# Optimization experiments

Hardware: AMD Instinct MI355X
Metric: run time of the kernel (lower is better)

The kernel has to match this reference:

```python
import jax, jax.numpy as jnp
import numpy as np

B, S, H, HKV, D = 1, 1024, 32, 8, 128
HID = H * D
GROUPS = H // HKV
ALPHA_K, ALPHA_V = 0.5, 0.5
GAMMA_MIN, GAMMA_MAX = 0.5, 2.0
ETA_MIN, ETA_MAX = 0.5, 2.0
BETA_BIAS, BIAS_CAP = 1.0, 5.0
BETA_POST = 0.5
ROPE_THETA = 10000.0


def setup_inputs() -> dict:
    key = jax.random.key(0)
    ks = jax.random.split(key, 9)
    hidden_states = jax.random.normal(ks[0], (B, S, HID), jnp.float32) * 0.02
    # additive causal mask (LLaMA-style, large negative above diagonal)
    causal = jnp.tril(jnp.ones((S, S), dtype=bool))
    attention_mask = jnp.where(causal, 0.0, -1e9).astype(jnp.float32)[None, None]
    position_ids = jnp.arange(S, dtype=jnp.int32)[None]
    sq = 1.0 / np.sqrt(HID)
    Wq = jax.random.normal(ks[1], (HID, HID), jnp.float32) * sq
    Wk = jax.random.normal(ks[2], (HKV * D, HID), jnp.float32) * sq
    Wv = jax.random.normal(ks[3], (HKV * D, HID), jnp.float32) * sq
    Wo = jax.random.normal(ks[4], (HID, HID), jnp.float32) * sq
    prior = jax.random.uniform(ks[5], (S,), jnp.float32)  # per-key-position prior, in [0,1)
    head_mask_l1 = (jax.random.uniform(ks[6], (H,)) > 0.5).astype(jnp.float32)
    head_mask_l2 = (jax.random.uniform(ks[7], (H,)) > 0.5).astype(jnp.float32)
    return {"hidden_states": hidden_states, "attention_mask": attention_mask,
            "position_ids": position_ids, "Wq": Wq, "Wk": Wk, "Wv": Wv, "Wo": Wo,
            "prior": prior, "head_mask_l1": head_mask_l1, "head_mask_l2": head_mask_l2}


def _rope(position_ids):
    inv_freq = 1.0 / (ROPE_THETA ** (jnp.arange(0, D, 2, dtype=jnp.float32) / D))
    freqs = position_ids.astype(jnp.float32)[..., None] * inv_freq  # [B,S,D/2]
    emb = jnp.concatenate([freqs, freqs], axis=-1)                  # [B,S,D]
    return jnp.cos(emb)[:, None], jnp.sin(emb)[:, None]             # [B,1,S,D]


def _rotate_half(x):
    x1, x2 = x[..., : D // 2], x[..., D // 2:]
    return jnp.concatenate([-x2, x1], axis=-1)


def reference(hidden_states, attention_mask, position_ids, Wq, Wk, Wv, Wo,
              prior, head_mask_l1, head_mask_l2):
    b, s, _ = hidden_states.shape
    # projections (Linear without bias: x @ W.T)
    q = (hidden_states @ Wq.T).reshape(b, s, H, D).transpose(0, 2, 1, 3)     # [B,H,S,D]
    k = (hidden_states @ Wk.T).reshape(b, s, HKV, D).transpose(0, 2, 1, 3)   # [B,Hkv,S,D]
    v = (hidden_states @ Wv.T).reshape(b, s, HKV, D).transpose(0, 2, 1, 3)
    cos, sin = _rope(position_ids)
    q = q * cos + _rotate_half(q) * sin
    k = k * cos + _rotate_half(k) * sin
    # repeat_kv: expand KV heads to match query heads (GQA)
    k = jnp.repeat(k, GROUPS, axis=1)  # [B,H,S,D]
    v = jnp.repeat(v, GROUPS, axis=1)
    # level4_scale: per-key-position multiplicative scaling of K and V
    gamma = jnp.clip(1.0 + ALPHA_K * prior, GAMMA_MIN, GAMMA_MAX)  # [S]
    eta = jnp.clip(1.0 + ALPHA_V * prior, ETA_MIN, ETA_MAX)
    k = k * gamma[None, None, :, None]
    v = v * eta[None, None, :, None]
    # attention logits
    attn = jnp.einsum('bhqd,bhkd->bhqk', q, k) / np.sqrt(D)
    # level1_bias: capped additive bias on logits, blended per-head
    bias = jnp.clip(BETA_BIAS * prior, -BIAS_CAP, BIAS_CAP)        # [S] over key dim
    steered = attn + bias[None, None, None, :]
    attn = attn + (steered - attn) * head_mask_l1[None, :, None, None]
    # causal mask
    attn = attn + attention_mask
    probs = jax.nn.softmax(attn.astype(jnp.float32), axis=-1)
    # level2_post: post-softmax rescale + renormalize, blended per-head
    sp = probs * (1.0 + BETA_POST * prior)[None, None, None, :]
    sp = sp / jnp.sum(sp, axis=-1, keepdims=True)
    probs = probs + (sp - probs) * head_mask_l2[None, :, None, None]
    out = jnp.einsum('bhqk,bhkd->bhqd', probs, v)                  # [B,H,S,D]
    out = out.transpose(0, 2, 1, 3).reshape(b, s, HID)
    return out @ Wo.T
```

## Files before the change

### kernel.cpp

```cpp
#include <hip/hip_runtime.h>
#include <math.h>

#define S_LEN 1024
#define HID_DIM 4096
#define NH 32
#define NKV 8
#define DH 128

typedef __attribute__((ext_vector_type(8))) short sh8;
typedef __attribute__((ext_vector_type(4))) short sh4;
typedef __attribute__((ext_vector_type(4))) float f4;

__device__ __forceinline__ unsigned short f2bf(float x) {
    union { float f; unsigned int u; } v; v.f = x;
    unsigned int r = v.u + 0x7FFFu + ((v.u >> 16) & 1u);
    return (unsigned short)(r >> 16);
}

__device__ __forceinline__ void gl_lds16(const unsigned short* g, unsigned short* l) {
    __builtin_amdgcn_global_load_lds(
        (const __attribute__((address_space(1))) unsigned int*)g,
        (__attribute__((address_space(3))) unsigned int*)l, 16, 0, 0);
}


__global__ void cvt_hw(const float* __restrict__ hidden, const float* __restrict__ Wq,
                       const float* __restrict__ Wk, const float* __restrict__ Wv,
                       unsigned short* __restrict__ hbf, unsigned short* __restrict__ wbuf)
{
    const int idx = blockIdx.x * 256 + threadIdx.x;
    const int NH4 = (S_LEN * HID_DIM) / 4;
    float4 v;
    sh4* dst;
    if (idx < NH4) {
        v = ((const float4*)hidden)[idx];
        dst = (sh4*)hbf + idx;
    } else {
        const int j = idx - NH4;
        const int row = j >> 10;
        if (row < 4096)      v = ((const float4*)Wq)[j];
        else if (row < 5120) v = ((const float4*)Wk)[j - 4096 * 1024];
        else                 v = ((const float4*)Wv)[j - 5120 * 1024];
        dst = (sh4*)wbuf + j;
    }
    sh4 o;
    o.x = (short)f2bf(v.x); o.y = (short)f2bf(v.y);
    o.z = (short)f2bf(v.z); o.w = (short)f2bf(v.w);
    *dst = o;
}

__global__ __launch_bounds__(256)
void gemm_t(const unsigned short* __restrict__ A, const unsigned short* __restrict__ B,
            float* __restrict__ C, int K, int ldc)
{
    __shared__ __attribute__((aligned(16))) unsigned short sA[2][2][64 * 32];
    __shared__ __attribute__((aligned(16))) unsigned short sB[2][2][128 * 32];

    const int tid  = threadIdx.x;
    const int wave = tid >> 6;
    const int lane = tid & 63;
    const int l15  = lane & 15;
    const int quad = lane >> 4;
    const int m0   = blockIdx.y * 64;
    const int n0   = blockIdx.x * 128;
    const int wm   = (wave >> 1) * 32;
    const int wn   = (wave & 1) * 64;

    const int sslot = (lane & 7) ^ ((lane >> 3) & 7);
    const int srow  = 2 * (lane >> 3) + (sslot >> 2);
    const int scol  = (sslot & 3) * 8;

    const unsigned short* Ag  = A + (size_t)(m0 + 16 * wave + srow) * K + scol;
    const unsigned short* Bg1 = B + (size_t)(n0 + 16 * wave + srow) * K + scol;
    const unsigned short* Bg2 = B + (size_t)(n0 + 64 + 16 * wave + srow) * K + scol;

    f4 acc[2][4];
#pragma unroll
    for (int i = 0; i < 2; i++)
#pragma unroll
        for (int j = 0; j < 4; j++)
            acc[i][j] = f4{0.0f, 0.0f, 0.0f, 0.0f};

    const int rphys = ((((l15 & 1) << 2) + quad) ^ (l15 >> 1)) * 8;

#pragma unroll
    for (int s = 0; s < 2; s++) {
        gl_lds16(Ag + 32 * s,  &sA[0][s][wave * 512]);
        gl_lds16(Bg1 + 32 * s, &sB[0][s][wave * 512]);
        gl_lds16(Bg2 + 32 * s, &sB[0][s][2048 + wave * 512]);
    }

    for (int k0 = 0; k0 < K; k0 += 64) {
        const int cur = (k0 >> 6) & 1;
        __syncthreads();
        const int k1 = k0 + 64;
        if (k1 < K) {
#pragma unroll
            for (int s = 0; s < 2; s++) {
                gl_lds16(Ag + k1 + 32 * s,  &sA[cur ^ 1][s][wave * 512]);
                gl_lds16(Bg1 + k1 + 32 * s, &sB[cur ^ 1][s][wave * 512]);
                gl_lds16(Bg2 + k1 + 32 * s, &sB[cur ^ 1][s][2048 + wave * 512]);
            }
        }

#pragma unroll
        for (int s = 0; s < 2; s++) {
            sh8 af[2], bf[4];
#pragma unroll
            for (int i = 0; i < 2; i++)
                af[i] = *(const sh8*)(&sA[cur][s][((wm + i * 16 + l15) >> 1) * 64 + rphys]);
#pragma unroll
            for (int j = 0; j < 4; j++)
                bf[j] = *(const sh8*)(&sB[cur][s][((wn + j * 16 + l15) >> 1) * 64 + rphys]);
#pragma unroll
            for (int i = 0; i < 2; i++)
#pragma unroll
                for (int j = 0; j < 4; j++)
                    acc[i][j] = __builtin_amdgcn_mfma_f32_16x16x32_bf16(af[i], bf[j], acc[i][j], 0, 0, 0);
        }
    }

#pragma unroll
    for (int i = 0; i < 2; i++) {
        const int mrow = m0 + wm + i * 16 + quad * 4;
#pragma unroll
        for (int j = 0; j < 4; j++) {
            const int ncol = n0 + wn + j * 16 + l15;
#pragma unroll
            for (int r = 0; r < 4; r++)
                C[(size_t)(mrow + r) * ldc + ncol] = acc[i][j][r];
        }
    }
}

__global__ void prep2(const float* __restrict__ qkv, const int* __restrict__ pos_ids,
                      const float* __restrict__ prior,
                      const float* __restrict__ Wo,
                      unsigned short* __restrict__ Qb, unsigned short* __restrict__ Kb,
                      unsigned short* __restrict__ Vt, float* __restrict__ addvT,
                      unsigned short* __restrict__ Wob)
{
    const int idx = blockIdx.x * blockDim.x + threadIdx.x;
    const int NQ = S_LEN * 40 * 64;
    const int NV = S_LEN * NKV * DH;
    if (idx < NQ) {
        const int s   = idx / (40 * 64);
        const int rem = idx % (40 * 64);
        const int hh  = rem >> 6;
        const int i   = rem & 63;
        const float pos  = (float)pos_ids[s];
        const float invf = exp2f(-13.287712379549449f * (i * 0.015625f));
        const float ph = pos * invf;
        const float c = cosf(ph), sn = sinf(ph);
        if (hh < NH) {
            const float* base = qkv + (size_t)s * 6144 + hh * 128;
            const float x1 = base[i], x2 = base[i + 64];
            const float sc = 0.08838834764831845f * 1.4426950408889634f;
            unsigned short* q = Qb + ((size_t)hh * S_LEN + s) * DH;
            q[i]      = f2bf((x1 * c - x2 * sn) * sc);
            q[i + 64] = f2bf((x2 * c + x1 * sn) * sc);
        } else {
            const int kvh = hh - NH;
            const float* base = qkv + (size_t)s * 6144 + 4096 + kvh * 128;
            const float p = prior[s];
            const float gamma = fminf(fmaxf(1.0f + 0.5f * p, 0.5f), 2.0f);
            const float x1 = base[i], x2 = base[i + 64];
            unsigned short* kp = Kb + ((size_t)kvh * S_LEN + s) * DH;
            kp[i]      = f2bf((x1 * c - x2 * sn) * gamma);
            kp[i + 64] = f2bf((x2 * c + x1 * sn) * gamma);
        }
    } else if (idx < NQ + NV) {
        const int j = idx - NQ;
        const int s   = j / (NKV * DH);
        const int rem = j % (NKV * DH);
        const int kvh = rem >> 7;
        const int d   = rem & 127;
        const float p = prior[s];
        const float eta = fminf(fmaxf(1.0f + 0.5f * p, 0.5f), 2.0f);
        const float val = qkv[(size_t)s * 6144 + 5120 + kvh * 128 + d] * eta;
        Vt[((size_t)kvh * DH + d) * S_LEN + s] = f2bf(val);
    } else {
        const int j2 = idx - NQ - NV;
        if (j2 < 4 * S_LEN) {
            const int c = j2 >> 10;
            const int s = j2 & 1023;
            const float p = prior[s];
            const float bias = fminf(fmaxf(p, -5.0f), 5.0f);
            float v = 0.0f;
            if (c & 1) v += bias;
            if (c & 2) v += log1pf(0.5f * p);
            addvT[j2] = v * 1.4426950408889634f;
        } else {
            const int j3 = j2 - 4 * S_LEN;
            if (j3 < (HID_DIM * HID_DIM) / 4) {
                const float4 v = ((const float4*)Wo)[j3];
                sh4 o;
                o.x = (short)f2bf(v.x); o.y = (short)f2bf(v.y);
                o.z = (short)f2bf(v.z); o.w = (short)f2bf(v.w);
                ((sh4*)Wob)[j3] = o;
            }
        }
    }
}

__global__ __launch_bounds__(256)
void attn5(const unsigned short* __restrict__ Qb, const unsigned short* __restrict__ Kb,
           const unsigned short* __restrict__ Vt, const float* __restrict__ addvT,
           const float* __restrict__ hm1, const float* __restrict__ hm2,
           unsigned short* __restrict__ ctx)
{
    __shared__ __attribute__((aligned(16))) unsigned short sK[2][32 * 128];
    __shared__ __attribute__((aligned(16))) unsigned short sV[2][128 * 32];
    __shared__ __attribute__((aligned(16))) short sP[4][16 * 40];

    const int h    = blockIdx.x;
    const int qb   = (gridDim.y - 1) - blockIdx.y;
    const int tid  = threadIdx.x;
    const int wave = tid >> 6;
    const int lane = tid & 63;
    const int l15  = lane & 15;
    const int quad = lane >> 4;
    const int q0   = qb * 64 + wave * 16;
    const int kvh  = h >> 2;
    const int combo = (hm1[h] > 0.5f ? 1 : 0) + (hm2[h] > 0.5f ? 2 : 0);
    const float* av = addvT + combo * S_LEN;

    const unsigned short* ksrcE = Kb + ((size_t)kvh * S_LEN + (lane >> 4)) * DH
                                  + (((lane & 15) ^ (lane >> 4)) * 8);
    const unsigned short* ksrcO = Kb + ((size_t)kvh * S_LEN + (lane >> 4)) * DH
                                  + (((lane & 15) ^ (4 + (lane >> 4))) * 8);
    const unsigned short* vsrc0 = Vt + ((size_t)kvh * DH + (lane >> 2)) * S_LEN
                                  + (((lane & 3) ^ ((lane >> 2) & 3)) * 8);

    auto stage = [&](int c, int buf) {
        const int k0 = c * 32;
        if (wave < 2) {
#pragma unroll
            for (int j = 0; j < 4; j++) {
                const int i = wave * 4 + j;
                const unsigned short* src = (j & 1) ? ksrcO : ksrcE;
                gl_lds16(src + (size_t)(k0 + 4 * i) * DH, &sK[buf][i * 512]);
            }
        } else {
#pragma unroll
            for (int j = 0; j < 4; j++) {
                const int i = (wave - 2) * 4 + j;
                gl_lds16(vsrc0 + (size_t)(16 * i) * S_LEN + k0, &sV[buf][i * 512]);
            }
        }
    };

    sh8 qf[4];
    {
        const unsigned short* qbase = Qb + ((size_t)h * S_LEN + q0 + l15) * DH + quad * 8;
#pragma unroll
        for (int kc = 0; kc < 4; kc++)
            qf[kc] = *(const sh8*)(qbase + kc * 32);
    }

    f4 O[8];
#pragma unroll
    for (int dt = 0; dt < 8; dt++) O[dt] = f4{0.0f, 0.0f, 0.0f, 0.0f};
    float lrun[4] = {0.0f, 0.0f, 0.0f, 0.0f};

    short* pl = &sP[wave][0];
    const int sw = l15 & 7;
    const int sv = l15 & 3;
    const int nch = 2 * qb + 2;

    stage(0, 0);

    for (int c = 0; c < nch; c++) {
        const int cur = c & 1;
        const int k0 = c * 32;
        __syncthreads();
        if (c + 1 < nch) stage(c + 1, cur ^ 1);

#pragma unroll
        for (int t = 0; t < 2; t++) {
            f4 a = f4{0.0f, 0.0f, 0.0f, 0.0f};
            __builtin_amdgcn_s_setprio(1);
#pragma unroll
            for (int kc = 0; kc < 4; kc++) {
                const sh8 kfr = *(const sh8*)(&sK[cur][(t * 16 + l15) * 128 + ((kc * 4 + quad) ^ sw) * 8]);
                a = __builtin_amdgcn_mfma_f32_16x16x32_bf16(qf[kc], kfr, a, 0, 0, 0);
            }
            __builtin_amdgcn_s_setprio(0);
            const int key = k0 + t * 16 + l15;
            const float ad = av[key];
#pragma unroll
            for (int r = 0; r < 4; r++) {
                const int qrow = q0 + quad * 4 + r;
                float ex = exp2f(a[r] + ad);
                ex = (key <= qrow) ? ex : 0.0f;
                lrun[r] += ex;
                pl[(quad * 4 + r) * 40 + t * 16 + l15] = (short)f2bf(ex);
            }
        }
        asm volatile("s_waitcnt lgkmcnt(0)" ::: "memory");
        const sh8 ap = *(const sh8*)(&pl[l15 * 40 + quad * 8]);
        __builtin_amdgcn_s_setprio(1);
#pragma unroll
        for (int dt = 0; dt < 8; dt++) {
            const sh8 vfr = *(const sh8*)(&sV[cur][(dt * 16 + l15) * 32 + (quad ^ sv) * 8]);
            O[dt] = __builtin_amdgcn_mfma_f32_16x16x32_bf16(ap, vfr, O[dt], 0, 0, 0);
        }
        __builtin_amdgcn_s_setprio(0);
    }

#pragma unroll
    for (int r = 0; r < 4; r++) {
        float l = lrun[r];
        l += __shfl_xor(l, 1); l += __shfl_xor(l, 2);
        l += __shfl_xor(l, 4); l += __shfl_xor(l, 8);
        const float inv = 1.0f / l;
        const int row = q0 + quad * 4 + r;
        unsigned short* cp = ctx + (size_t)row * HID_DIM + h * DH;
#pragma unroll
        for (int dt = 0; dt < 8; dt++)
            cp[dt * 16 + l15] = f2bf(O[dt][r] * inv);
    }
}


#define LDSW 40

__global__ __launch_bounds__(256)
void gemm_bt(const float* __restrict__ A,
             const float* __restrict__ B0, const float* __restrict__ B1,
             const float* __restrict__ B2, int n_b1, int n_b2,
             float* __restrict__ C, int M, int N, int K, int ldc)
{
    __shared__ __attribute__((aligned(16))) short sA[128 * LDSW];
    __shared__ __attribute__((aligned(16))) short sB[128 * LDSW];
    const int tid  = threadIdx.x;
    const int m0   = blockIdx.y * 128;
    const int n0   = blockIdx.x * 128;
    const float* Bp = B0; int nloc = n0;
    if (n0 >= n_b2)      { Bp = B2; nloc = n0 - n_b2; }
    else if (n0 >= n_b1) { Bp = B1; nloc = n0 - n_b1; }
    const int wave = tid >> 6, lane = tid & 63;
    const int l15 = lane & 15, quad = lane >> 4;
    const int wm = (wave >> 1) * 64, wn = (wave & 1) * 64;
    const int rb = tid >> 3, c4 = (tid & 7) * 4;
    f4 acc[4][4];
#pragma unroll
    for (int i = 0; i < 4; i++)
#pragma unroll
        for (int j = 0; j < 4; j++) acc[i][j] = f4{0.0f, 0.0f, 0.0f, 0.0f};
    for (int k0 = 0; k0 < K; k0 += 32) {
        __syncthreads();
#pragma unroll
        for (int i = 0; i < 4; i++) {
            const int row = rb + 32 * i;
            const float4 va = *(const float4*)(A  + (size_t)(m0 + row) * K + k0 + c4);
            const float4 vb = *(const float4*)(Bp + (size_t)(nloc + row) * K + k0 + c4);
            sh4 sa, sb;
            sa.x = (short)f2bf(va.x); sa.y = (short)f2bf(va.y);
            sa.z = (short)f2bf(va.z); sa.w = (short)f2bf(va.w);
            sb.x = (short)f2bf(vb.x); sb.y = (short)f2bf(vb.y);
            sb.z = (short)f2bf(vb.z); sb.w = (short)f2bf(vb.w);
            *(sh4*)(&sA[row * LDSW + c4]) = sa;
            *(sh4*)(&sB[row * LDSW + c4]) = sb;
        }
        __syncthreads();
        sh8 af[4], bf[4];
#pragma unroll
        for (int i = 0; i < 4; i++) af[i] = *(const sh8*)(&sA[(wm + i * 16 + l15) * LDSW + quad * 8]);
#pragma unroll
        for (int j = 0; j < 4; j++) bf[j] = *(const sh8*)(&sB[(wn + j * 16 + l15) * LDSW + quad * 8]);
#pragma unroll
        for (int i = 0; i < 4; i++)
#pragma unroll
            for (int j = 0; j < 4; j++)
                acc[i][j] = __builtin_amdgcn_mfma_f32_16x16x32_bf16(af[i], bf[j], acc[i][j], 0, 0, 0);
    }
#pragma unroll
    for (int i = 0; i < 4; i++) {
        const int mrow = m0 + wm + i * 16 + quad * 4;
#pragma unroll
        for (int j = 0; j < 4; j++) {
            const int ncol = n0 + wn + j * 16 + l15;
#pragma unroll
            for (int r = 0; r < 4; r++)
                C[(size_t)(mrow + r) * ldc + ncol] = acc[i][j][r];
        }
    }
}

__global__ void prep_rope(const float* __restrict__ qkv, const int* __restrict__ pos_ids,
                          const float* __restrict__ prior,
                          unsigned short* __restrict__ Qb, unsigned short* __restrict__ Kb,
                          unsigned short* __restrict__ Vt)
{
    const int idx = blockIdx.x * blockDim.x + threadIdx.x;
    const int NQ = S_LEN * 40 * 64;
    if (idx < NQ) {
        const int s = idx / (40 * 64);
        const int rem = idx % (40 * 64);
        const int hh = rem >> 6, i = rem & 63;
        const float pos = (float)pos_ids[s];
        const float invf = exp2f(-13.287712379549449f * (i * 0.015625f));
        const float ph = pos * invf;
        const float c = cosf(ph), sn = sinf(ph);
        if (hh < NH) {
            const float* base = qkv + (size_t)s * 6144 + hh * 128;
            const float x1 = base[i], x2 = base[i + 64];
            const float sc = 0.08838834764831845f;
            unsigned short* q = Qb + ((size_t)hh * S_LEN + s) * DH;
            q[i] = f2bf((x1 * c - x2 * sn) * sc);
            q[i + 64] = f2bf((x2 * c + x1 * sn) * sc);
        } else {
            const int kvh = hh - NH;
            const float* base = qkv + (size_t)s * 6144 + 4096 + kvh * 128;
            const float p = prior[s];
            const float gamma = fminf(fmaxf(1.0f + 0.5f * p, 0.5f), 2.0f);
            const float x1 = base[i], x2 = base[i + 64];
            unsigned short* kp = Kb + ((size_t)kvh * S_LEN + s) * DH;
            kp[i] = f2bf((x1 * c - x2 * sn) * gamma);
            kp[i + 64] = f2bf((x2 * c + x1 * sn) * gamma);
        }
    } else {
        const int j = idx - NQ;
        if (j < S_LEN * NKV * DH) {
            const int s = j / (NKV * DH);
            const int rem = j % (NKV * DH);
            const int kvh = rem >> 7, d = rem & 127;
            const float p = prior[s];
            const float eta = fminf(fmaxf(1.0f + 0.5f * p, 0.5f), 2.0f);
            const float val = qkv[(size_t)s * 6144 + 5120 + kvh * 128 + d] * eta;
            Vt[((size_t)kvh * DH + d) * S_LEN + s] = f2bf(val);
        }
    }
}

__global__ __launch_bounds__(256)
void attn_kernel(const unsigned short* __restrict__ Qb, const unsigned short* __restrict__ Kb,
                 const unsigned short* __restrict__ Vt, const float* __restrict__ prior,
                 const float* __restrict__ hm1, const float* __restrict__ hm2,
                 float* __restrict__ ctx)
{
    __shared__ __attribute__((aligned(16))) short p_lds[4][16 * LDSW];
    const int h = blockIdx.x, qb = blockIdx.y;
    const int wave = threadIdx.x >> 6, lane = threadIdx.x & 63;
    const int l15 = lane & 15, quad = lane >> 4;
    const int q0 = qb * 64 + wave * 16;
    const int kvh = h >> 2;
    const float m1 = hm1[h], m2 = hm2[h];
    const float NEG = -3.0e38f;
    sh8 qf[4];
    {
        const unsigned short* qbase = Qb + ((size_t)h * S_LEN + q0 + l15) * DH + quad * 8;
#pragma unroll
        for (int kc = 0; kc < 4; kc++) qf[kc] = *(const sh8*)(qbase + kc * 32);
    }
    f4 O[8];
#pragma unroll
    for (int dt = 0; dt < 8; dt++) O[dt] = f4{0.0f, 0.0f, 0.0f, 0.0f};
    float mrun[4], lrun[4];
#pragma unroll
    for (int r = 0; r < 4; r++) { mrun[r] = NEG; lrun[r] = 0.0f; }
    short* pl = &p_lds[wave][0];
    const int qmax = q0 + 15;
    for (int key0 = 0; key0 <= qmax; key0 += 32) {
        float sc[2][4];
#pragma unroll
        for (int t = 0; t < 2; t++) {
            const int kt = key0 + t * 16;
            const unsigned short* kb = Kb + ((size_t)kvh * S_LEN + kt + l15) * DH + quad * 8;
            f4 a = f4{0.0f, 0.0f, 0.0f, 0.0f};
#pragma unroll
            for (int kc = 0; kc < 4; kc++) {
                const sh8 bfr = *(const sh8*)(kb + kc * 32);
                a = __builtin_amdgcn_mfma_f32_16x16x32_bf16(qf[kc], bfr, a, 0, 0, 0);
            }
            const int key = kt + l15;
            const float p = prior[key];
            const float bias = fminf(fmaxf(p, -5.0f), 5.0f);
            const float addv = m1 * bias + m2 * logf(1.0f + 0.5f * p);
#pragma unroll
            for (int r = 0; r < 4; r++) {
                const int qrow = q0 + quad * 4 + r;
                sc[t][r] = (key <= qrow) ? (a[r] + addv) : NEG;
            }
        }
        float cm[4], mnew[4], alpha[4], rs[4];
#pragma unroll
        for (int r = 0; r < 4; r++) {
            cm[r] = fmaxf(sc[0][r], sc[1][r]);
            cm[r] = fmaxf(cm[r], __shfl_xor(cm[r], 1));
            cm[r] = fmaxf(cm[r], __shfl_xor(cm[r], 2));
            cm[r] = fmaxf(cm[r], __shfl_xor(cm[r], 4));
            cm[r] = fmaxf(cm[r], __shfl_xor(cm[r], 8));
            mnew[r] = fmaxf(mrun[r], cm[r]);
            alpha[r] = expf(mrun[r] - mnew[r]);
        }
        float e[2][4];
#pragma unroll
        for (int t = 0; t < 2; t++)
#pragma unroll
            for (int r = 0; r < 4; r++) e[t][r] = expf(sc[t][r] - mnew[r]);
#pragma unroll
        for (int r = 0; r < 4; r++) {
            rs[r] = e[0][r] + e[1][r];
            rs[r] += __shfl_xor(rs[r], 1); rs[r] += __shfl_xor(rs[r], 2);
            rs[r] += __shfl_xor(rs[r], 4); rs[r] += __shfl_xor(rs[r], 8);
            lrun[r] = lrun[r] * alpha[r] + rs[r];
            mrun[r] = mnew[r];
        }
#pragma unroll
        for (int dt = 0; dt < 8; dt++)
#pragma unroll
            for (int r = 0; r < 4; r++) O[dt][r] *= alpha[r];
#pragma unroll
        for (int t = 0; t < 2; t++)
#pragma unroll
            for (int r = 0; r < 4; r++)
                pl[(quad * 4 + r) * LDSW + t * 16 + l15] = (short)f2bf(e[t][r]);
        asm volatile("s_waitcnt lgkmcnt(0)" ::: "memory");
        const sh8 ap = *(const sh8*)(&pl[l15 * LDSW + quad * 8]);
        const unsigned short* vb = Vt + ((size_t)kvh * DH + l15) * S_LEN + key0 + quad * 8;
#pragma unroll
        for (int dt = 0; dt < 8; dt++) {
            const sh8 bfv = *(const sh8*)(vb + (size_t)dt * 16 * S_LEN);
            O[dt] = __builtin_amdgcn_mfma_f32_16x16x32_bf16(ap, bfv, O[dt], 0, 0, 0);
        }
    }
#pragma unroll
    for (int r = 0; r < 4; r++) {
        const float inv = 1.0f / lrun[r];
        const int row = q0 + quad * 4 + r;
        float* cp = ctx + (size_t)row * HID_DIM + h * DH;
#pragma unroll
        for (int dt = 0; dt < 8; dt++) cp[dt * 16 + l15] = O[dt][r] * inv;
    }
}


extern "C" void kernel_launch(void* const* d_in, const int* in_sizes, int n_in,
                              void* d_out, int out_size, void* d_ws, size_t ws_size,
                              hipStream_t stream)
{
    const float* hidden  = (const float*)d_in[0];
    const int*   pos_ids = (const int*)d_in[2];
    const float* Wq = (const float*)d_in[3];
    const float* Wk = (const float*)d_in[4];
    const float* Wv = (const float*)d_in[5];
    const float* Wo = (const float*)d_in[6];
    const float* prior = (const float*)d_in[7];
    const float* hm1 = (const float*)d_in[8];
    const float* hm2 = (const float*)d_in[9];
    float* out = (float*)d_out;
    char* ws = (char*)d_ws;

    const size_t FAST_NEED = 96485376ull;
    if (ws_size >= FAST_NEED) {
        unsigned short* Wbuf = (unsigned short*)ws;
        unsigned short* Cbf  = (unsigned short*)(ws + 33554432);
        unsigned short* Hbf  = (unsigned short*)(ws + 50331648);
        float*          qkv  = (float*)(ws + 58720256);
        unsigned short* Qb   = (unsigned short*)(ws + 83886080);
        unsigned short* Kb   = (unsigned short*)(ws + 92274688);
        unsigned short* Vt   = (unsigned short*)(ws + 94371840);
        float*          addv = (float*)(ws + 96468992);

        cvt_hw<<<28672, 256, 0, stream>>>(hidden, Wq, Wk, Wv, Hbf, Wbuf);
        gemm_t<<<dim3(48, 16), 256, 0, stream>>>(Hbf, Wbuf, qkv, 4096, 6144);
        prep2<<<30736, 256, 0, stream>>>(qkv, pos_ids, prior, Wo, Qb, Kb, Vt, addv, Wbuf);
        attn5<<<dim3(32, 16), 256, 0, stream>>>(Qb, Kb, Vt, addv, hm1, hm2, Cbf);
        gemm_t<<<dim3(32, 16), 256, 0, stream>>>(Cbf, Wbuf, out, 4096, 4096);
    } else {
        float*          qkv = (float*)ws;
        float*          ctx = (float*)(ws + 25165824);
        unsigned short* Qb  = (unsigned short*)(ws + 41943040);
        unsigned short* Kb  = (unsigned short*)(ws + 50331648);
        unsigned short* Vt  = (unsigned short*)(ws + 52428800);
        gemm_bt<<<dim3(48, 8), 256, 0, stream>>>(hidden, Wq, Wk, Wv, 4096, 5120,
                                                 qkv, 1024, 6144, 4096, 6144);
        prep_rope<<<14336, 256, 0, stream>>>(qkv, pos_ids, prior, Qb, Kb, Vt);
        attn_kernel<<<dim3(32, 16), 256, 0, stream>>>(Qb, Kb, Vt, prior, hm1, hm2, ctx);
        gemm_bt<<<dim3(32, 8), 256, 0, stream>>>(ctx, Wo, Wo, Wo, 1 << 30, 1 << 30,
                                                 out, 1024, 4096, 4096, 4096);
    }
}
```

Before: 373.4 us.

## Use 4-stage LDS ring with explicit vmcnt waits in projection GEMM

Replaces the double-buffered 64-wide K pipeline in gemm_t with a 4-slot ring of 32-wide K stages, keeping three stages of global→LDS loads in flight. Partial s_waitcnt vmcnt counts plus raw s_barrier replace the full __syncthreads drain. The aim is to hide global load latency better behind MFMA work. In exchange it depends on exact vmcnt accounting (three loads per stage), and the loop tail is unrolled by hand.

```diff
diff --git a/kernel.cpp b/kernel.cpp
--- a/kernel.cpp
+++ b/kernel.cpp
@@ -53,8 +53,8 @@
 void gemm_t(const unsigned short* __restrict__ A, const unsigned short* __restrict__ B,
             float* __restrict__ C, int K, int ldc)
 {
-    __shared__ __attribute__((aligned(16))) unsigned short sA[2][2][64 * 32];
-    __shared__ __attribute__((aligned(16))) unsigned short sB[2][2][128 * 32];
+    __shared__ __attribute__((aligned(16))) unsigned short sA[4][64 * 32];
+    __shared__ __attribute__((aligned(16))) unsigned short sB[4][128 * 32];
 
     const int tid  = threadIdx.x;
     const int wave = tid >> 6;
@@ -83,42 +83,44 @@
 
     const int rphys = ((((l15 & 1) << 2) + quad) ^ (l15 >> 1)) * 8;
 
-#pragma unroll
-    for (int s = 0; s < 2; s++) {
-        gl_lds16(Ag + 32 * s,  &sA[0][s][wave * 512]);
-        gl_lds16(Bg1 + 32 * s, &sB[0][s][wave * 512]);
-        gl_lds16(Bg2 + 32 * s, &sB[0][s][2048 + wave * 512]);
-    }
-
-    for (int k0 = 0; k0 < K; k0 += 64) {
-        const int cur = (k0 >> 6) & 1;
-        __syncthreads();
-        const int k1 = k0 + 64;
-        if (k1 < K) {
-#pragma unroll
-            for (int s = 0; s < 2; s++) {
-                gl_lds16(Ag + k1 + 32 * s,  &sA[cur ^ 1][s][wave * 512]);
-                gl_lds16(Bg1 + k1 + 32 * s, &sB[cur ^ 1][s][wave * 512]);
-                gl_lds16(Bg2 + k1 + 32 * s, &sB[cur ^ 1][s][2048 + wave * 512]);
-            }
-        }
-
-#pragma unroll
-        for (int s = 0; s < 2; s++) {
-            sh8 af[2], bf[4];
-#pragma unroll
-            for (int i = 0; i < 2; i++)
-                af[i] = *(const sh8*)(&sA[cur][s][((wm + i * 16 + l15) >> 1) * 64 + rphys]);
+    const int NS = K >> 5;
+
+    auto stage = [&](int s) {
+        const int b = s & 3;
+        gl_lds16(Ag  + 32 * s, &sA[b][wave * 512]);
+        gl_lds16(Bg1 + 32 * s, &sB[b][wave * 512]);
+        gl_lds16(Bg2 + 32 * s, &sB[b][2048 + wave * 512]);
+    };
+    auto compute = [&](int s) {
+        const int b = s & 3;
+        sh8 af[2], bf[4];
+#pragma unroll
+        for (int i = 0; i < 2; i++)
+            af[i] = *(const sh8*)(&sA[b][((wm + i * 16 + l15) >> 1) * 64 + rphys]);
+#pragma unroll
+        for (int j = 0; j < 4; j++)
+            bf[j] = *(const sh8*)(&sB[b][((wn + j * 16 + l15) >> 1) * 64 + rphys]);
+#pragma unroll
+        for (int i = 0; i < 2; i++)
 #pragma unroll
             for (int j = 0; j < 4; j++)
-                bf[j] = *(const sh8*)(&sB[cur][s][((wn + j * 16 + l15) >> 1) * 64 + rphys]);
-#pragma unroll
-            for (int i = 0; i < 2; i++)
-#pragma unroll
-                for (int j = 0; j < 4; j++)
-                    acc[i][j] = __builtin_amdgcn_mfma_f32_16x16x32_bf16(af[i], bf[j], acc[i][j], 0, 0, 0);
-        }
-    }
+                acc[i][j] = __builtin_amdgcn_mfma_f32_16x16x32_bf16(af[i], bf[j], acc[i][j], 0, 0, 0);
+    };
+
+    stage(0); stage(1); stage(2);
+
+    for (int i = 0; i < NS - 2; i++) {
+        asm volatile("s_waitcnt vmcnt(6)" ::: "memory");
+        __builtin_amdgcn_s_barrier();
+        if (i + 3 < NS) stage(i + 3);
+        compute(i);
+    }
+    asm volatile("s_waitcnt vmcnt(3)" ::: "memory");
+    __builtin_amdgcn_s_barrier();
+    compute(NS - 2);
+    asm volatile("s_waitcnt vmcnt(0)" ::: "memory");
+    __builtin_amdgcn_s_barrier();
+    compute(NS - 1);
 
 #pragma unroll
     for (int i = 0; i < 2; i++) {
```

Measured after the change: 396.5 us. 1.06x slower.

## Load K and V fragments directly from global memory instead of LDS staging

Applied to the files above, without the earlier changes.

Removes the double-buffered LDS staging of K and V tiles (global_load_lds plus __syncthreads) in the attention kernel. Each wave now reads its MFMA K and V fragments straight from global memory, relying on L1/L2 for reuse across the four waves. This drops block-wide barriers and LDS traffic, but each wave now issues redundant global loads with no prefetch overlap, which can expose memory latency.

```diff
diff --git a/kernel.cpp b/kernel.cpp
--- a/kernel.cpp
+++ b/kernel.cpp
@@ -209,8 +209,6 @@
            const float* __restrict__ hm1, const float* __restrict__ hm2,
            unsigned short* __restrict__ ctx)
 {
-    __shared__ __attribute__((aligned(16))) unsigned short sK[2][32 * 128];
-    __shared__ __attribute__((aligned(16))) unsigned short sV[2][128 * 32];
     __shared__ __attribute__((aligned(16))) short sP[4][16 * 40];
 
     const int h    = blockIdx.x;
@@ -225,31 +223,6 @@
     const int combo = (hm1[h] > 0.5f ? 1 : 0) + (hm2[h] > 0.5f ? 2 : 0);
     const float* av = addvT + combo * S_LEN;
 
-    const unsigned short* ksrcE = Kb + ((size_t)kvh * S_LEN + (lane >> 4)) * DH
-                                  + (((lane & 15) ^ (lane >> 4)) * 8);
-    const unsigned short* ksrcO = Kb + ((size_t)kvh * S_LEN + (lane >> 4)) * DH
-                                  + (((lane & 15) ^ (4 + (lane >> 4))) * 8);
-    const unsigned short* vsrc0 = Vt + ((size_t)kvh * DH + (lane >> 2)) * S_LEN
-                                  + (((lane & 3) ^ ((lane >> 2) & 3)) * 8);
-
-    auto stage = [&](int c, int buf) {
-        const int k0 = c * 32;
-        if (wave < 2) {
-#pragma unroll
-            for (int j = 0; j < 4; j++) {
-                const int i = wave * 4 + j;
-                const unsigned short* src = (j & 1) ? ksrcO : ksrcE;
-                gl_lds16(src + (size_t)(k0 + 4 * i) * DH, &sK[buf][i * 512]);
-            }
-        } else {
-#pragma unroll
-            for (int j = 0; j < 4; j++) {
-                const int i = (wave - 2) * 4 + j;
-                gl_lds16(vsrc0 + (size_t)(16 * i) * S_LEN + k0, &sV[buf][i * 512]);
-            }
-        }
-    };
-
     sh8 qf[4];
     {
         const unsigned short* qbase = Qb + ((size_t)h * S_LEN + q0 + l15) * DH + quad * 8;
@@ -264,25 +237,22 @@
     float lrun[4] = {0.0f, 0.0f, 0.0f, 0.0f};
 
     short* pl = &sP[wave][0];
-    const int sw = l15 & 7;
-    const int sv = l15 & 3;
     const int nch = 2 * qb + 2;
 
-    stage(0, 0);
+    const unsigned short* kbase = Kb + ((size_t)kvh * S_LEN + l15) * DH + quad * 8;
+    const unsigned short* vbase = Vt + ((size_t)kvh * DH + l15) * S_LEN + quad * 8;
 
     for (int c = 0; c < nch; c++) {
-        const int cur = c & 1;
         const int k0 = c * 32;
-        __syncthreads();
-        if (c + 1 < nch) stage(c + 1, cur ^ 1);
 
 #pragma unroll
         for (int t = 0; t < 2; t++) {
+            const unsigned short* kb = kbase + (size_t)(k0 + t * 16) * DH;
             f4 a = f4{0.0f, 0.0f, 0.0f, 0.0f};
             __builtin_amdgcn_s_setprio(1);
 #pragma unroll
             for (int kc = 0; kc < 4; kc++) {
-                const sh8 kfr = *(const sh8*)(&sK[cur][(t * 16 + l15) * 128 + ((kc * 4 + quad) ^ sw) * 8]);
+                const sh8 kfr = *(const sh8*)(kb + kc * 32);
                 a = __builtin_amdgcn_mfma_f32_16x16x32_bf16(qf[kc], kfr, a, 0, 0, 0);
             }
             __builtin_amdgcn_s_setprio(0);
@@ -302,7 +272,7 @@
         __builtin_amdgcn_s_setprio(1);
 #pragma unroll
         for (int dt = 0; dt < 8; dt++) {
-            const sh8 vfr = *(const sh8*)(&sV[cur][(dt * 16 + l15) * 32 + (quad ^ sv) * 8]);
+            const sh8 vfr = *(const sh8*)(vbase + (size_t)dt * 16 * S_LEN + k0);
             O[dt] = __builtin_amdgcn_mfma_f32_16x16x32_bf16(ap, vfr, O[dt], 0, 0, 0);
         }
         __builtin_amdgcn_s_setprio(0);
```

New measurement: 452.8 us. +21.3%, slower.
